# Kernel tuning notes

Measured on AMD Instinct MI355X. Metric: run time of the kernel, lower is better.

The kernel has to match this reference:

```python
import jax, jax.numpy as jnp
import numpy as np

HIDDEN = 1024
NUM_HEADS = 16
HEAD_DIM = HIDDEN // NUM_HEADS  # 64
B, LQ, LK = 2, 2048, 2048


def setup_inputs() -> dict:
    key = jax.random.key(0)
    ks = jax.random.split(key, 9)
    s = 1.0 / np.sqrt(HIDDEN)
    return {
        "hidden_states_query": jax.random.normal(ks[0], (B, LQ, HIDDEN), jnp.float32),
        "hidden_states_key": jax.random.normal(ks[1], (B, LK, HIDDEN), jnp.float32),
        "attention_mask": jnp.ones((B, LQ, LK), jnp.float32),
        "Wq": jax.random.normal(ks[2], (HIDDEN, HIDDEN), jnp.float32) * s,
        "bq": jax.random.normal(ks[3], (HIDDEN,), jnp.float32) * s,
        "Wk": jax.random.normal(ks[4], (HIDDEN, HIDDEN), jnp.float32) * s,
        "bk": jax.random.normal(ks[5], (HIDDEN,), jnp.float32) * s,
        "Wv": jax.random.normal(ks[6], (HIDDEN, HIDDEN), jnp.float32) * s,
        "bv": jax.random.normal(ks[7], (HIDDEN,), jnp.float32) * s,
    }


def _split_heads(x):
    # [B, L, H*D] -> [B, nH, L, D]
    b, l, _ = x.shape
    return x.reshape(b, l, NUM_HEADS, HEAD_DIM).transpose(0, 2, 1, 3)


def reference(hidden_states_query, hidden_states_key, attention_mask, Wq, bq, Wk, bk, Wv, bv):
    # nn.Linear applies x @ W.T + b; weights here stored as [out, in]
    q = _split_heads(hidden_states_query @ Wq.T + bq)
    k = _split_heads(hidden_states_key @ Wk.T + bk)
    v = _split_heads(hidden_states_key @ Wv.T + bv)
    scale = 1.0 / np.sqrt(HEAD_DIM)
    scores = jnp.einsum("bhqd,bhkd->bhqk", q * scale, k)  # [B, nH, Lq, Lk]
    # mask: 1 -> 0, 0 -> -10000, broadcast over heads
    scores = scores + ((1.0 - attention_mask) * -10000.0)[:, None, :, :]
    probs = jax.nn.softmax(scores, axis=-1)
    ctx = jnp.einsum("bhqk,bhkd->bhqd", probs, v)
    b, h, lq, d = ctx.shape
    return ctx.transpose(0, 2, 1, 3).reshape(b, lq, h * d)
```

## Files before the change

### kernel.cpp

```cpp
#include <hip/hip_runtime.h>
#include <hip/hip_bf16.h>

#define HID 1024
#define NH 16
#define HD 64
#define SEQ 2048
#define NB 2
#define NTOK (NB * SEQ)

typedef __attribute__((ext_vector_type(8))) short bf16x8;
typedef __attribute__((ext_vector_type(4))) float f32x4;
typedef __attribute__((ext_vector_type(4))) unsigned u32x4;

#define QSCALE 0.18033688011112042f
#define MASKSCALE 1.4426950408889634f

__device__ __forceinline__ unsigned short f2bf(float f) {
    unsigned u = __builtin_bit_cast(unsigned, f);
    u += 0x7FFFu + ((u >> 16) & 1u);
    return (unsigned short)(u >> 16);
}
__device__ __forceinline__ unsigned cvtpk(float a, float b) {
    unsigned r;
    asm("v_cvt_pk_bf16_f32 %0, %1, %2" : "=v"(r) : "v"(a), "v"(b));
    return r;
}
__device__ __forceinline__ void gload_lds16(const unsigned short* g, unsigned short* l) {
    __builtin_amdgcn_global_load_lds(
        (const __attribute__((address_space(1))) unsigned int*)g,
        (__attribute__((address_space(3))) unsigned int*)l, 16, 0, 0);
}

__global__ __launch_bounds__(256) void cvt_all(
    const float* __restrict__ xq, const float* __restrict__ xk,
    const float* __restrict__ Wq, const float* __restrict__ Wk, const float* __restrict__ Wv,
    const float* __restrict__ mask,
    unsigned short* __restrict__ dxq, unsigned short* __restrict__ dxk,
    unsigned short* __restrict__ dwq, unsigned short* __restrict__ dwk,
    unsigned short* __restrict__ dwv, int* __restrict__ flags) {
    const int id = blockIdx.x;
    if (id >= 11264) {
        const int lane = threadIdx.x & 63;
        int i = ((id - 11264) * 256 + threadIdx.x) * 4;
        float4 v = *(const float4*)(mask + i);
        bool ok = (v.x == 1.0f) && (v.y == 1.0f) && (v.z == 1.0f) && (v.w == 1.0f);
        unsigned long long bal = __ballot(ok);
        int g = lane >> 4;
        if ((lane & 15) == 0) {
            unsigned m16 = (unsigned)(bal >> (g * 16)) & 0xFFFFu;
            if (m16 != 0xFFFFu) {
                int b = i >> 22;
                int rem = i & 4194303;
                int q = rem >> 11, k = rem & 2047;
                atomicAnd(&flags[(b << 10) + ((q >> 6) << 5) + (k >> 6)], 0);
            }
        }
        return;
    }
    const float* src;
    unsigned short* dst;
    int base;
    float scale = 1.0f;
    if (id < 4096)       { src = xq; dst = dxq; base = 0; }
    else if (id < 8192)  { src = xk; dst = dxk; base = 4096; }
    else if (id < 9216)  { src = Wq; dst = dwq; base = 8192; scale = QSCALE; }
    else if (id < 10240) { src = Wk; dst = dwk; base = 9216; }
    else                 { src = Wv; dst = dwv; base = 10240; }
    int i = ((id - base) * 256 + threadIdx.x) * 4;
    float4 v = *(const float4*)(src + i);
    ushort4 o;
    o.x = f2bf(v.x * scale); o.y = f2bf(v.y * scale);
    o.z = f2bf(v.z * scale); o.w = f2bf(v.w * scale);
    *(ushort4*)(dst + i) = o;
}

__global__ __launch_bounds__(256) void proj_gemm(
    const unsigned short* __restrict__ xq, const unsigned short* __restrict__ xk,
    const unsigned short* __restrict__ wq, const unsigned short* __restrict__ wk,
    const unsigned short* __restrict__ wv,
    const float* __restrict__ bq, const float* __restrict__ bk, const float* __restrict__ bv,
    unsigned short* __restrict__ Qh, unsigned short* __restrict__ Kh,
    unsigned short* __restrict__ Vt) {
    __shared__ __align__(16) unsigned short As[2][128 * 32];
    __shared__ __align__(16) unsigned short Bs[2][128 * 32];

    const int z = blockIdx.z;
    const unsigned short *A, *B;
    const float* bias;
    float bsc;
    unsigned short* out;
    int mt, nt;
    bool tr;
    if (z == 0)      { A = xq; B = wq; bias = bq; bsc = QSCALE; out = Qh; tr = false; mt = blockIdx.x; nt = blockIdx.y; }
    else if (z == 1) { A = xk; B = wk; bias = bk; bsc = 1.0f;  out = Kh; tr = false; mt = blockIdx.x; nt = blockIdx.y; }
    else             { A = wv; B = xk; bias = bv; bsc = 1.0f;  out = Vt; tr = true;
                       mt = blockIdx.x & 7; nt = blockIdx.y * 4 + (blockIdx.x >> 3); }
    const int m0 = mt * 128, n0 = nt * 128;
    const int tid = threadIdx.x, wave = tid >> 6, lane = tid & 63;
    const int wr = (wave >> 1) * 64, wc = (wave & 1) * 64;
    const int frow = lane & 15, fk = (lane >> 4) * 8;
    const int srow = lane >> 2, skb = (lane & 3) * 8;

    const unsigned short* Ab = A + (size_t)(m0 + wave * 16 + srow) * HID + skb;
    const unsigned short* Bb = B + (size_t)(n0 + wave * 16 + srow) * HID + skb;

    f32x4 acc[4][4] = {};

#define PSTAGE(bi, k0)                                                                 \
    do {                                                                               \
        gload_lds16(Ab + (k0), &As[bi][wave * 512]);                                   \
        gload_lds16(Ab + (size_t)64 * HID + (k0), &As[bi][2048 + wave * 512]);         \
        gload_lds16(Bb + (k0), &Bs[bi][wave * 512]);                                   \
        gload_lds16(Bb + (size_t)64 * HID + (k0), &Bs[bi][2048 + wave * 512]);         \
    } while (0)

    PSTAGE(0, 0);
    __syncthreads();
    int buf = 0;

    for (int it = 0; it < 32; ++it) {
        if (it < 31) PSTAGE(buf ^ 1, (it + 1) * 32);
        bf16x8 af[4], bfr[4];
#pragma unroll
        for (int i = 0; i < 4; ++i) af[i] = *(const bf16x8*)&As[buf][(wr + i * 16 + frow) * 32 + fk];
#pragma unroll
        for (int j = 0; j < 4; ++j) bfr[j] = *(const bf16x8*)&Bs[buf][(wc + j * 16 + frow) * 32 + fk];
        __builtin_amdgcn_s_setprio(1);
#pragma unroll
        for (int i = 0; i < 4; ++i)
#pragma unroll
            for (int j = 0; j < 4; ++j)
                acc[i][j] = __builtin_amdgcn_mfma_f32_16x16x32_bf16(af[i], bfr[j], acc[i][j], 0, 0, 0);
        __builtin_amdgcn_s_setprio(0);
        if (it < 31) {
            __syncthreads();
            buf ^= 1;
        }
    }

#pragma unroll
    for (int i = 0; i < 4; ++i)
#pragma unroll
        for (int j = 0; j < 4; ++j)
#pragma unroll
            for (int r = 0; r < 4; ++r) {
                int row = m0 + wr + i * 16 + (lane >> 4) * 4 + r;
                int col = n0 + wc + j * 16 + frow;
                float v = acc[i][j][r];
                if (!tr) {
                    v += bsc * bias[col];
                    int b = row >> 11, l = row & 2047, hh = col >> 6, d = col & 63;
                    out[(((size_t)(b * NH + hh)) * SEQ + l) * HD + d] = f2bf(v);
                } else {
                    v += bias[row];
                    int b = col >> 11, ll = col & 2047, hh = row >> 6, d = row & 63;
                    int lp = (ll & ~0x1C) | ((ll & 0x0C) << 1) | ((ll & 0x10) >> 2);
                    out[(((size_t)(b * NH + hh)) * HD + d) * SEQ + lp] = f2bf(v);
                }
            }
#undef PSTAGE
}

__global__ __launch_bounds__(256) void flash_attn(
    const unsigned short* __restrict__ Qh, const unsigned short* __restrict__ Kh,
    const unsigned short* __restrict__ Vt, const float* __restrict__ mask,
    const int* __restrict__ flags, float* __restrict__ out) {
    __shared__ __align__(16) unsigned short Ks[2][64 * 64];
    __shared__ __align__(16) unsigned short Vs[2][64 * 64];

    const int tid = threadIdx.x, wave = tid >> 6, lane = tid & 63;
    const int id = blockIdx.x;
    const int bh = (id & 7) * 4 + ((id >> 3) & 3);
    const int qi = id >> 5;
    const int b = bh >> 4, h = bh & 15;
    const size_t hoff = (size_t)bh * SEQ * HD;
    const int fr = lane & 15, hi = lane >> 4;
    const int f7 = fr & 7, swz3 = f7 << 3;
    const int qa = qi * 64 + wave * 16 + fr;

    bf16x8 qfa0 = *(const bf16x8*)&Qh[hoff + (size_t)qa * HD + hi * 8];
    bf16x8 qfa1 = *(const bf16x8*)&Qh[hoff + (size_t)qa * HD + 32 + hi * 8];

    const float* mrowA = mask + (size_t)b * SEQ * SEQ + (size_t)qa * SEQ;
    const int* frow = flags + (b << 10) + (qi << 5);
    int fv = frow[lane & 31];
    const unsigned long long bm = __ballot(fv != 0);

    const int srow = wave * 8 + (lane >> 3);
    const int sch = (lane & 7) ^ (srow & 7);
    const unsigned short* kbase = Kh + hoff + (size_t)srow * HD + (sch << 3);
    const unsigned short* vbase = Vt + hoff + (size_t)srow * SEQ + (sch << 3);

    f32x4 accA[4] = {};
    f32x4 laccA = {};
    const bf16x8 ones = {0x3F80, 0x3F80, 0x3F80, 0x3F80, 0x3F80, 0x3F80, 0x3F80, 0x3F80};

#define STAGE(bi, t)                                                              \
    do {                                                                          \
        gload_lds16(kbase + (size_t)(t) * 64 * HD, &Ks[bi][(wave * 8) * 64]);     \
        gload_lds16(kbase + (size_t)((t) * 64 + 32) * HD,                         \
                    &Ks[bi][(wave * 8 + 32) * 64]);                               \
        gload_lds16(vbase + (t) * 64, &Vs[bi][(wave * 8) * 64]);                  \
        gload_lds16(vbase + (size_t)32 * SEQ + (t) * 64,                          \
                    &Vs[bi][(wave * 8 + 32) * 64]);                               \
    } while (0)

    STAGE(0, 0);
    __syncthreads();
    int buf = 0;

    for (int t = 0; t < 32; ++t) {
        if (t < 31) STAGE(buf ^ 1, t + 1);
        const unsigned short* ks = Ks[buf];
        const unsigned short* vs = Vs[buf];

        f32x4 sA[4];
        __builtin_amdgcn_s_setprio(1);
#pragma unroll
        for (int sub = 0; sub < 4; ++sub) {
            const int rbase = (sub * 16 + fr) * 64;
            bf16x8 kf0 = *(const bf16x8*)&ks[rbase + ((hi << 3) ^ swz3)];
            bf16x8 kf1 = *(const bf16x8*)&ks[rbase + (((hi + 4) << 3) ^ swz3)];
            f32x4 z = {0.f, 0.f, 0.f, 0.f};
            z = __builtin_amdgcn_mfma_f32_16x16x32_bf16(kf0, qfa0, z, 0, 0, 0);
            z = __builtin_amdgcn_mfma_f32_16x16x32_bf16(kf1, qfa1, z, 0, 0, 0);
            sA[sub] = z;
        }
        __builtin_amdgcn_s_setprio(0);

        if (!((bm >> t) & 1)) {
            const int k0 = t * 64;
#pragma unroll
            for (int sub = 0; sub < 4; ++sub) {
                float4 ma = *(const float4*)&mrowA[k0 + sub * 16 + hi * 4];
                sA[sub][0] += (1.f - ma.x) * (-10000.f * MASKSCALE);
                sA[sub][1] += (1.f - ma.y) * (-10000.f * MASKSCALE);
                sA[sub][2] += (1.f - ma.z) * (-10000.f * MASKSCALE);
                sA[sub][3] += (1.f - ma.w) * (-10000.f * MASKSCALE);
            }
        }

#pragma unroll
        for (int sub = 0; sub < 4; ++sub)
#pragma unroll
            for (int r = 0; r < 4; ++r)
                sA[sub][r] = __builtin_amdgcn_exp2f(sA[sub][r]);

        u32x4 w0, w1;
        w0[0] = cvtpk(sA[0][0], sA[0][1]); w0[1] = cvtpk(sA[0][2], sA[0][3]);
        w0[2] = cvtpk(sA[1][0], sA[1][1]); w0[3] = cvtpk(sA[1][2], sA[1][3]);
        w1[0] = cvtpk(sA[2][0], sA[2][1]); w1[1] = cvtpk(sA[2][2], sA[2][3]);
        w1[2] = cvtpk(sA[3][0], sA[3][1]); w1[3] = cvtpk(sA[3][2], sA[3][3]);
        bf16x8 pA0 = __builtin_bit_cast(bf16x8, w0);
        bf16x8 pA1 = __builtin_bit_cast(bf16x8, w1);

        __builtin_amdgcn_s_setprio(1);
        laccA = __builtin_amdgcn_mfma_f32_16x16x32_bf16(ones, pA0, laccA, 0, 0, 0);
        laccA = __builtin_amdgcn_mfma_f32_16x16x32_bf16(ones, pA1, laccA, 0, 0, 0);

#pragma unroll
        for (int sub = 0; sub < 4; ++sub) {
            const int rbase = (sub * 16 + fr) * 64;
            bf16x8 vf0 = *(const bf16x8*)&vs[rbase + ((hi << 3) ^ swz3)];
            bf16x8 vf1 = *(const bf16x8*)&vs[rbase + (((hi + 4) << 3) ^ swz3)];
            accA[sub] = __builtin_amdgcn_mfma_f32_16x16x32_bf16(vf0, pA0, accA[sub], 0, 0, 0);
            accA[sub] = __builtin_amdgcn_mfma_f32_16x16x32_bf16(vf1, pA1, accA[sub], 0, 0, 0);
        }
        __builtin_amdgcn_s_setprio(0);

        if (t < 31) {
            __syncthreads();
            buf ^= 1;
        }
    }

    float rA = 1.0f / laccA[0];
#pragma unroll
    for (int sub = 0; sub < 4; ++sub) {
        float4 oA = {accA[sub][0] * rA, accA[sub][1] * rA, accA[sub][2] * rA, accA[sub][3] * rA};
        *(float4*)&out[((size_t)b * SEQ + qa) * HID + h * HD + sub * 16 + hi * 4] = oA;
    }
#undef STAGE
}

extern "C" void kernel_launch(void* const* d_in, const int* in_sizes, int n_in,
                              void* d_out, int out_size, void* d_ws, size_t ws_size,
                              hipStream_t stream) {
    const float* xq = (const float*)d_in[0];
    const float* xk = (const float*)d_in[1];
    const float* mask = (const float*)d_in[2];
    const float* Wq = (const float*)d_in[3];
    const float* bq = (const float*)d_in[4];
    const float* Wk = (const float*)d_in[5];
    const float* bk = (const float*)d_in[6];
    const float* Wv = (const float*)d_in[7];
    const float* bv = (const float*)d_in[8];
    float* out = (float*)d_out;

    const size_t NX = (size_t)NTOK * HID;
    const size_t NW = (size_t)HID * HID;
    const size_t need = (5 * NX + 3 * NW) * sizeof(unsigned short) + 2048 * sizeof(int);
    if (ws_size < need) return;

    unsigned short* ws = (unsigned short*)d_ws;
    unsigned short* xq_b = ws;
    unsigned short* xk_b = xq_b + NX;
    unsigned short* wq_b = xk_b + NX;
    unsigned short* wk_b = wq_b + NW;
    unsigned short* wv_b = wk_b + NW;
    unsigned short* Qh = wv_b + NW;
    unsigned short* Kh = Qh + NX;
    unsigned short* Vt = Kh + NX;
    int* flags = (int*)(Vt + NX);

    hipMemsetAsync(flags, 0xFF, 2048 * sizeof(int), stream);
    cvt_all<<<19456, 256, 0, stream>>>(xq, xk, Wq, Wk, Wv, mask,
                                       xq_b, xk_b, wq_b, wk_b, wv_b, flags);
    proj_gemm<<<dim3(32, 8, 3), 256, 0, stream>>>(xq_b, xk_b, wq_b, wk_b, wv_b,
                                                  bq, bk, bv, Qh, Kh, Vt);
    flash_attn<<<1024, 256, 0, stream>>>(Qh, Kh, Vt, mask, flags, out);
}
```

Before: 120.5 us.

## Triple-buffer LDS pipelines with vmcnt waits, swizzle GEMM LDS, remap GEMM grid

Both the projection GEMM and flash attention move from double-buffered staging with __syncthreads to a three-stage ring, prefetching two tiles ahead and waiting with partial s_waitcnt vmcnt plus a raw s_barrier. The GEMM also XOR-swizzles its LDS layout to reduce bank conflicts and uses a flattened 1D grid remapped so consecutive blocks spread across XCDs. Launch bounds request 3 blocks per CU. The aim is to hide global-load latency and cut sync stalls, at the cost of more LDS per block, which may limit occupancy.

```diff
diff --git a/kernel.cpp b/kernel.cpp
--- a/kernel.cpp
+++ b/kernel.cpp
@@ -14,6 +14,8 @@
 
 #define QSCALE 0.18033688011112042f
 #define MASKSCALE 1.4426950408889634f
+
+#define MFMA16(a, b, c) __builtin_amdgcn_mfma_f32_16x16x32_bf16((a), (b), (c), 0, 0, 0)
 
 __device__ __forceinline__ unsigned short f2bf(float f) {
     unsigned u = __builtin_bit_cast(unsigned, f);
@@ -74,69 +76,83 @@
     *(ushort4*)(dst + i) = o;
 }
 
-__global__ __launch_bounds__(256) void proj_gemm(
+__global__ __launch_bounds__(256, 3) void proj_gemm(
     const unsigned short* __restrict__ xq, const unsigned short* __restrict__ xk,
     const unsigned short* __restrict__ wq, const unsigned short* __restrict__ wk,
     const unsigned short* __restrict__ wv,
     const float* __restrict__ bq, const float* __restrict__ bk, const float* __restrict__ bv,
     unsigned short* __restrict__ Qh, unsigned short* __restrict__ Kh,
     unsigned short* __restrict__ Vt) {
-    __shared__ __align__(16) unsigned short As[2][128 * 32];
-    __shared__ __align__(16) unsigned short Bs[2][128 * 32];
-
-    const int z = blockIdx.z;
+    __shared__ __align__(16) unsigned short As[3][128 * 32];
+    __shared__ __align__(16) unsigned short Bs[3][128 * 32];
+
+    const int id = blockIdx.x;
+    const int xid = (id & 7) * 96 + (id >> 3);
     const unsigned short *A, *B;
     const float* bias;
-    float bsc;
+    float bsc = 1.0f;
     unsigned short* out;
     int mt, nt;
-    bool tr;
-    if (z == 0)      { A = xq; B = wq; bias = bq; bsc = QSCALE; out = Qh; tr = false; mt = blockIdx.x; nt = blockIdx.y; }
-    else if (z == 1) { A = xk; B = wk; bias = bk; bsc = 1.0f;  out = Kh; tr = false; mt = blockIdx.x; nt = blockIdx.y; }
-    else             { A = wv; B = xk; bias = bv; bsc = 1.0f;  out = Vt; tr = true;
-                       mt = blockIdx.x & 7; nt = blockIdx.y * 4 + (blockIdx.x >> 3); }
+    bool tr = false;
+    if (xid < 256)      { A = xq; B = wq; bias = bq; bsc = QSCALE; out = Qh;
+                          mt = xid >> 3; nt = xid & 7; }
+    else if (xid < 512) { A = xk; B = wk; bias = bk; out = Kh;
+                          mt = (xid - 256) >> 3; nt = (xid - 256) & 7; }
+    else                { A = wv; B = xk; bias = bv; out = Vt; tr = true;
+                          mt = (xid - 512) & 7; nt = (xid - 512) >> 3; }
     const int m0 = mt * 128, n0 = nt * 128;
     const int tid = threadIdx.x, wave = tid >> 6, lane = tid & 63;
     const int wr = (wave >> 1) * 64, wc = (wave & 1) * 64;
-    const int frow = lane & 15, fk = (lane >> 4) * 8;
-    const int srow = lane >> 2, skb = (lane & 3) * 8;
-
-    const unsigned short* Ab = A + (size_t)(m0 + wave * 16 + srow) * HID + skb;
-    const unsigned short* Bb = B + (size_t)(n0 + wave * 16 + srow) * HID + skb;
+    const int fr = lane & 15, hi = lane >> 4;
+
+    const int uswz = (hi ^ ((fr >> 1) & 3)) << 3;
+    const int abase = (wr + fr) * 32 + uswz;
+    const int bbase = (wc + fr) * 32 + uswz;
+
+    const int srow = wave * 16 + (lane >> 2);
+    const int sunit = (lane & 3) ^ ((lane >> 3) & 3);
+    const unsigned short* Asrc = A + (size_t)(m0 + srow) * HID + sunit * 8;
+    const unsigned short* Bsrc = B + (size_t)(n0 + srow) * HID + sunit * 8;
+
+    unsigned short *cA = As[0], *nA = As[1], *fA = As[2];
+    unsigned short *cB = Bs[0], *nB = Bs[1], *fB = Bs[2];
 
     f32x4 acc[4][4] = {};
 
-#define PSTAGE(bi, k0)                                                                 \
-    do {                                                                               \
-        gload_lds16(Ab + (k0), &As[bi][wave * 512]);                                   \
-        gload_lds16(Ab + (size_t)64 * HID + (k0), &As[bi][2048 + wave * 512]);         \
-        gload_lds16(Bb + (k0), &Bs[bi][wave * 512]);                                   \
-        gload_lds16(Bb + (size_t)64 * HID + (k0), &Bs[bi][2048 + wave * 512]);         \
+#define PSTG(t, ap, bp)                                                          \
+    do {                                                                         \
+        gload_lds16(Asrc + (t) * 32, (ap) + wave * 512);                         \
+        gload_lds16(Asrc + (size_t)64 * HID + (t) * 32, (ap) + 2048 + wave * 512); \
+        gload_lds16(Bsrc + (t) * 32, (bp) + wave * 512);                         \
+        gload_lds16(Bsrc + (size_t)64 * HID + (t) * 32, (bp) + 2048 + wave * 512); \
     } while (0)
 
-    PSTAGE(0, 0);
-    __syncthreads();
-    int buf = 0;
-
-    for (int it = 0; it < 32; ++it) {
-        if (it < 31) PSTAGE(buf ^ 1, (it + 1) * 32);
+    PSTG(0, cA, cB);
+    PSTG(1, nA, nB);
+
+    for (int t = 0; t < 32; ++t) {
+        if (t < 31) asm volatile("s_waitcnt vmcnt(4)" ::: "memory");
+        else        asm volatile("s_waitcnt vmcnt(0)" ::: "memory");
+        __builtin_amdgcn_s_barrier();
+        if (t < 30) PSTG(t + 2, fA, fB);
+
         bf16x8 af[4], bfr[4];
 #pragma unroll
-        for (int i = 0; i < 4; ++i) af[i] = *(const bf16x8*)&As[buf][(wr + i * 16 + frow) * 32 + fk];
-#pragma unroll
-        for (int j = 0; j < 4; ++j) bfr[j] = *(const bf16x8*)&Bs[buf][(wc + j * 16 + frow) * 32 + fk];
+        for (int i = 0; i < 4; ++i) af[i] = *(const bf16x8*)&cA[abase + i * 512];
+#pragma unroll
+        for (int j = 0; j < 4; ++j) bfr[j] = *(const bf16x8*)&cB[bbase + j * 512];
         __builtin_amdgcn_s_setprio(1);
 #pragma unroll
         for (int i = 0; i < 4; ++i)
 #pragma unroll
             for (int j = 0; j < 4; ++j)
-                acc[i][j] = __builtin_amdgcn_mfma_f32_16x16x32_bf16(af[i], bfr[j], acc[i][j], 0, 0, 0);
+                acc[i][j] = MFMA16(af[i], bfr[j], acc[i][j]);
         __builtin_amdgcn_s_setprio(0);
-        if (it < 31) {
-            __syncthreads();
-            buf ^= 1;
-        }
+
+        unsigned short* ta = cA; cA = nA; nA = fA; fA = ta;
+        unsigned short* tb = cB; cB = nB; nB = fB; fB = tb;
     }
+#undef PSTG
 
 #pragma unroll
     for (int i = 0; i < 4; ++i)
@@ -144,8 +160,8 @@
         for (int j = 0; j < 4; ++j)
 #pragma unroll
             for (int r = 0; r < 4; ++r) {
-                int row = m0 + wr + i * 16 + (lane >> 4) * 4 + r;
-                int col = n0 + wc + j * 16 + frow;
+                int row = m0 + wr + i * 16 + hi * 4 + r;
+                int col = n0 + wc + j * 16 + fr;
                 float v = acc[i][j][r];
                 if (!tr) {
                     v += bsc * bias[col];
@@ -158,15 +174,14 @@
                     out[(((size_t)(b * NH + hh)) * HD + d) * SEQ + lp] = f2bf(v);
                 }
             }
-#undef PSTAGE
-}
-
-__global__ __launch_bounds__(256) void flash_attn(
+}
+
+__global__ __launch_bounds__(256, 3) void flash_attn(
     const unsigned short* __restrict__ Qh, const unsigned short* __restrict__ Kh,
     const unsigned short* __restrict__ Vt, const float* __restrict__ mask,
     const int* __restrict__ flags, float* __restrict__ out) {
-    __shared__ __align__(16) unsigned short Ks[2][64 * 64];
-    __shared__ __align__(16) unsigned short Vs[2][64 * 64];
+    __shared__ __align__(16) unsigned short Ks[3][64 * 64];
+    __shared__ __align__(16) unsigned short Vs[3][64 * 64];
 
     const int tid = threadIdx.x, wave = tid >> 6, lane = tid & 63;
     const int id = blockIdx.x;
@@ -195,35 +210,36 @@
     f32x4 laccA = {};
     const bf16x8 ones = {0x3F80, 0x3F80, 0x3F80, 0x3F80, 0x3F80, 0x3F80, 0x3F80, 0x3F80};
 
-#define STAGE(bi, t)                                                              \
-    do {                                                                          \
-        gload_lds16(kbase + (size_t)(t) * 64 * HD, &Ks[bi][(wave * 8) * 64]);     \
-        gload_lds16(kbase + (size_t)((t) * 64 + 32) * HD,                         \
-                    &Ks[bi][(wave * 8 + 32) * 64]);                               \
-        gload_lds16(vbase + (t) * 64, &Vs[bi][(wave * 8) * 64]);                  \
-        gload_lds16(vbase + (size_t)32 * SEQ + (t) * 64,                          \
-                    &Vs[bi][(wave * 8 + 32) * 64]);                               \
+    unsigned short *cK = &Ks[0][0], *nK = &Ks[1][0], *fK = &Ks[2][0];
+    unsigned short *cV = &Vs[0][0], *nV = &Vs[1][0], *fV = &Vs[2][0];
+
+#define STG(t, kd, vd)                                                           \
+    do {                                                                         \
+        gload_lds16(kbase + (size_t)(t) * 64 * HD, (kd) + (wave * 8) * 64);      \
+        gload_lds16(kbase + (size_t)((t) * 64 + 32) * HD, (kd) + (wave * 8 + 32) * 64); \
+        gload_lds16(vbase + (t) * 64, (vd) + (wave * 8) * 64);                   \
+        gload_lds16(vbase + (size_t)32 * SEQ + (t) * 64, (vd) + (wave * 8 + 32) * 64); \
     } while (0)
 
-    STAGE(0, 0);
-    __syncthreads();
-    int buf = 0;
+    STG(0, cK, cV);
+    STG(1, nK, nV);
 
     for (int t = 0; t < 32; ++t) {
-        if (t < 31) STAGE(buf ^ 1, t + 1);
-        const unsigned short* ks = Ks[buf];
-        const unsigned short* vs = Vs[buf];
+        if (t < 31) asm volatile("s_waitcnt vmcnt(4)" ::: "memory");
+        else        asm volatile("s_waitcnt vmcnt(0)" ::: "memory");
+        __builtin_amdgcn_s_barrier();
+        if (t < 30) STG(t + 2, fK, fV);
 
         f32x4 sA[4];
         __builtin_amdgcn_s_setprio(1);
 #pragma unroll
         for (int sub = 0; sub < 4; ++sub) {
             const int rbase = (sub * 16 + fr) * 64;
-            bf16x8 kf0 = *(const bf16x8*)&ks[rbase + ((hi << 3) ^ swz3)];
-            bf16x8 kf1 = *(const bf16x8*)&ks[rbase + (((hi + 4) << 3) ^ swz3)];
+            bf16x8 kf0 = *(const bf16x8*)&cK[rbase + ((hi << 3) ^ swz3)];
+            bf16x8 kf1 = *(const bf16x8*)&cK[rbase + (((hi + 4) << 3) ^ swz3)];
             f32x4 z = {0.f, 0.f, 0.f, 0.f};
-            z = __builtin_amdgcn_mfma_f32_16x16x32_bf16(kf0, qfa0, z, 0, 0, 0);
-            z = __builtin_amdgcn_mfma_f32_16x16x32_bf16(kf1, qfa1, z, 0, 0, 0);
+            z = MFMA16(kf0, qfa0, z);
+            z = MFMA16(kf1, qfa1, z);
             sA[sub] = z;
         }
         __builtin_amdgcn_s_setprio(0);
@@ -255,24 +271,23 @@
         bf16x8 pA1 = __builtin_bit_cast(bf16x8, w1);
 
         __builtin_amdgcn_s_setprio(1);
-        laccA = __builtin_amdgcn_mfma_f32_16x16x32_bf16(ones, pA0, laccA, 0, 0, 0);
-        laccA = __builtin_amdgcn_mfma_f32_16x16x32_bf16(ones, pA1, laccA, 0, 0, 0);
+        laccA = MFMA16(ones, pA0, laccA);
+        laccA = MFMA16(ones, pA1, laccA);
 
 #pragma unroll
         for (int sub = 0; sub < 4; ++sub) {
             const int rbase = (sub * 16 + fr) * 64;
-            bf16x8 vf0 = *(const bf16x8*)&vs[rbase + ((hi << 3) ^ swz3)];
-            bf16x8 vf1 = *(const bf16x8*)&vs[rbase + (((hi + 4) << 3) ^ swz3)];
-            accA[sub] = __builtin_amdgcn_mfma_f32_16x16x32_bf16(vf0, pA0, accA[sub], 0, 0, 0);
-            accA[sub] = __builtin_amdgcn_mfma_f32_16x16x32_bf16(vf1, pA1, accA[sub], 0, 0, 0);
+            bf16x8 vf0 = *(const bf16x8*)&cV[rbase + ((hi << 3) ^ swz3)];
+            bf16x8 vf1 = *(const bf16x8*)&cV[rbase + (((hi + 4) << 3) ^ swz3)];
+            accA[sub] = MFMA16(vf0, pA0, accA[sub]);
+            accA[sub] = MFMA16(vf1, pA1, accA[sub]);
         }
         __builtin_amdgcn_s_setprio(0);
 
-        if (t < 31) {
-            __syncthreads();
-            buf ^= 1;
-        }
+        unsigned short* tk = cK; cK = nK; nK = fK; fK = tk;
+        unsigned short* tv = cV; cV = nV; nV = fV; fV = tv;
     }
+#undef STG
 
     float rA = 1.0f / laccA[0];
 #pragma unroll
@@ -280,7 +295,6 @@
         float4 oA = {accA[sub][0] * rA, accA[sub][1] * rA, accA[sub][2] * rA, accA[sub][3] * rA};
         *(float4*)&out[((size_t)b * SEQ + qa) * HID + h * HD + sub * 16 + hi * 4] = oA;
     }
-#undef STAGE
 }
 
 extern "C" void kernel_launch(void* const* d_in, const int* in_sizes, int n_in,
@@ -316,7 +330,7 @@
     hipMemsetAsync(flags, 0xFF, 2048 * sizeof(int), stream);
     cvt_all<<<19456, 256, 0, stream>>>(xq, xk, Wq, Wk, Wv, mask,
                                        xq_b, xk_b, wq_b, wk_b, wv_b, flags);
-    proj_gemm<<<dim3(32, 8, 3), 256, 0, stream>>>(xq_b, xk_b, wq_b, wk_b, wv_b,
-                                                  bq, bk, bv, Qh, Kh, Vt);
+    proj_gemm<<<768, 256, 0, stream>>>(xq_b, xk_b, wq_b, wk_b, wv_b,
+                                       bq, bk, bv, Qh, Kh, Vt);
     flash_attn<<<1024, 256, 0, stream>>>(Qh, Kh, Vt, mask, flags, out);
 }
```

Result: faster. 112.6 us (-6.5%).
